# Kernel optimization log

Measured on AMD Instinct MI355X. Metric: run time of the kernel, lower is better.

## Reference

```python
import jax, jax.numpy as jnp
import numpy as np

N_NODES = 40000
N_EDGES = 640000
H = 128
N_REL2 = 474  # 2 * n_rel
BN_EPS = 1e-5


def setup_inputs() -> dict:
    key = jax.random.key(0)
    k1, k2, k3, k4, k5 = jax.random.split(key, 5)
    ent_emb = jax.random.normal(k1, (N_NODES, H), dtype=jnp.float32)
    rel_emb = jax.random.normal(k2, (N_REL2, H), dtype=jnp.float32)
    neigh_w = jax.random.normal(k3, (H, H), dtype=jnp.float32) * (1.0 / np.sqrt(H))
    bn_gamma = jnp.ones((H,), dtype=jnp.float32)
    bn_beta = jnp.zeros((H,), dtype=jnp.float32)
    rel_id = jax.random.randint(k4, (N_EDGES,), 0, N_REL2, dtype=jnp.int64)
    dst = jax.random.randint(k5, (N_EDGES,), 0, N_NODES, dtype=jnp.int64)
    return {"ent_emb": ent_emb, "rel_emb": rel_emb, "neigh_w": neigh_w,
            "bn_gamma": bn_gamma, "bn_beta": bn_beta, "rel_id": rel_id, "dst": dst}


def reference(ent_emb, rel_emb, neigh_w, bn_gamma, bn_beta, rel_id, dst):
    # per-edge relation embedding (gather)            [E, H]
    e = rel_emb[rel_id]
    # e_dot_v: edge emb dot destination node emb      [E]
    s = jnp.einsum('eh,eh->e', e, ent_emb[dst])
    # edge_softmax: softmax of s over edges grouped by destination node
    smax = jax.ops.segment_max(s, dst, num_segments=N_NODES)  # [N]
    ex = jnp.exp(s - smax[dst])
    denom = jax.ops.segment_sum(ex, dst, num_segments=N_NODES)  # [N]
    norm = ex / denom[dst]                                       # [E]
    # copy_e + sum: weighted scatter-sum of edge embeddings to dst nodes
    neigh = jax.ops.segment_sum(e * norm[:, None], dst, num_segments=N_NODES)  # [N, H]
    # dense update: mm + BatchNorm1d (training-mode batch stats) + tanh
    h = neigh @ neigh_w
    mean = jnp.mean(h, axis=0)
    var = jnp.var(h, axis=0)
    h = (h - mean) * jax.lax.rsqrt(var + BN_EPS) * bn_gamma + bn_beta
    return jnp.tanh(h)
```

## Files before the change

kernel.cpp:

```cpp
#include <hip/hip_runtime.h>

#define N_NODES 40000
#define N_EDGES 640000
#define HD 128
#define N_REL2 474
#define BN_EPS 1e-5f
#define NB_SCAN ((N_NODES + 255) / 256)

__global__ __launch_bounds__(256) void k_hist(
        const int* __restrict__ dst, int* __restrict__ counts) {
    int e = blockIdx.x * 256 + threadIdx.x;
    if (e < N_EDGES) atomicAdd(counts + dst[e], 1);
}

__global__ __launch_bounds__(256) void k_scan_part(
        const int* __restrict__ counts, int* __restrict__ bsum) {
    __shared__ int ls[256];
    int t = threadIdx.x;
    int idx = blockIdx.x * 256 + t;
    ls[t] = (idx < N_NODES) ? counts[idx] : 0;
    __syncthreads();
    #pragma unroll
    for (int off = 128; off > 0; off >>= 1) {
        if (t < off) ls[t] += ls[t + off];
        __syncthreads();
    }
    if (t == 0) bsum[blockIdx.x] = ls[0];
}

__global__ __launch_bounds__(256) void k_scan_down(
        const int* __restrict__ counts, const int* __restrict__ bsum,
        int* __restrict__ row_off, int* __restrict__ cursor) {
    __shared__ int btop[256];
    __shared__ int ls[256];
    int t = threadIdx.x;
    btop[t] = (t < NB_SCAN) ? bsum[t] : 0;
    __syncthreads();
    #pragma unroll
    for (int off = 1; off < 256; off <<= 1) {
        int tmp = (t >= off) ? btop[t - off] : 0;
        __syncthreads();
        btop[t] += tmp;
        __syncthreads();
    }
    int blockoff = (blockIdx.x == 0) ? 0 : btop[blockIdx.x - 1];
    int idx = blockIdx.x * 256 + t;
    int v = (idx < N_NODES) ? counts[idx] : 0;
    ls[t] = v;
    __syncthreads();
    #pragma unroll
    for (int off = 1; off < 256; off <<= 1) {
        int tmp = (t >= off) ? ls[t - off] : 0;
        __syncthreads();
        ls[t] += tmp;
        __syncthreads();
    }
    int excl = ls[t] - v + blockoff;
    if (idx < N_NODES) {
        row_off[idx] = excl;
        cursor[idx] = excl;
    }
    if (idx == N_NODES) row_off[N_NODES] = N_EDGES;
}

__global__ __launch_bounds__(256) void k_edge_sort(
        const float* __restrict__ ent_emb, const float* __restrict__ R,
        const int* __restrict__ rel_id, const int* __restrict__ dst,
        int* __restrict__ cursor, float2* __restrict__ sorted_pr) {
    int t = threadIdx.x;
    int e = blockIdx.x * 16 + (t >> 4);
    if (e >= N_EDGES) return;
    int lam = t & 15;
    int r = rel_id[e], d = dst[e];
    const float4* rr = (const float4*)(R + (size_t)r * HD);
    const float4* ee = (const float4*)(ent_emb + (size_t)d * HD);
    float4 a0 = rr[lam * 2], a1 = rr[lam * 2 + 1];
    float4 b0 = ee[lam * 2], b1 = ee[lam * 2 + 1];
    float s = a0.x * b0.x + a0.y * b0.y + a0.z * b0.z + a0.w * b0.w
            + a1.x * b1.x + a1.y * b1.y + a1.z * b1.z + a1.w * b1.w;
    #pragma unroll
    for (int m = 8; m >= 1; m >>= 1) s += __shfl_xor(s, m, 64);
    if (lam == 0) {
        float p = __expf(s);
        int pos = atomicAdd(cursor + d, 1);
        sorted_pr[pos] = make_float2(p, __int_as_float(r));
    }
}

__global__ __launch_bounds__(128) void k_rw(
        const float* __restrict__ R, const float* __restrict__ W,
        float* __restrict__ RW) {
    __shared__ float row[HD];
    int r = blockIdx.x, c = threadIdx.x;
    row[c] = R[(size_t)r * HD + c];
    __syncthreads();
    float acc = 0.f;
    #pragma unroll 8
    for (int k = 0; k < HD; ++k) acc += row[k] * W[(size_t)k * HD + c];
    RW[(size_t)r * HD + c] = acc;
}

__global__ __launch_bounds__(256) void k_node_acc(
        const float* __restrict__ RW, const int* __restrict__ row_off,
        const float2* __restrict__ sorted_pr, float* __restrict__ h) {
    __shared__ __align__(8) float2 pr_s[4][64];
    int wave = threadIdx.x >> 6, lane = threadIdx.x & 63;
    int n = blockIdx.x * 4 + wave;
    if (n >= N_NODES) return;
    int beg = row_off[n], end = row_off[n + 1];
    int c4 = lane & 15, g = lane >> 4;
    float acc[8] = {};
    float lp = 0.f;
    const float4* RW4 = (const float4*)RW;
    for (int base = beg; base < end; base += 64) {
        int cnt = min(64, end - base);
        if (lane < cnt) pr_s[wave][lane] = sorted_pr[base + lane];
        for (int j0 = 0; j0 < cnt; j0 += 4) {
            int eidx = j0 + g;
            if (eidx < cnt) {
                float2 v = pr_s[wave][eidx];
                float p = v.x;
                int r = __float_as_int(v.y);
                const float4* rowp = RW4 + (size_t)r * 32 + c4 * 2;
                float4 w0 = rowp[0], w1 = rowp[1];
                lp += p;
                acc[0] += p * w0.x; acc[1] += p * w0.y;
                acc[2] += p * w0.z; acc[3] += p * w0.w;
                acc[4] += p * w1.x; acc[5] += p * w1.y;
                acc[6] += p * w1.z; acc[7] += p * w1.w;
            }
        }
    }
    #pragma unroll
    for (int m = 16; m <= 32; m <<= 1) {
        lp += __shfl_xor(lp, m, 64);
        #pragma unroll
        for (int k = 0; k < 8; ++k) acc[k] += __shfl_xor(acc[k], m, 64);
    }
    float invl = (lp > 0.f) ? 1.f / lp : 0.f;
    if (g == 0) {
        float4* op = (float4*)(h + (size_t)n * HD + c4 * 8);
        op[0] = make_float4(acc[0] * invl, acc[1] * invl, acc[2] * invl, acc[3] * invl);
        op[1] = make_float4(acc[4] * invl, acc[5] * invl, acc[6] * invl, acc[7] * invl);
    }
}

__global__ __launch_bounds__(256) void k_stats(
        const float* __restrict__ Hout, float* __restrict__ colsum,
        float* __restrict__ colsumsq) {
    __shared__ float ls[256], lq[256];
    int t = threadIdx.x;
    int c = t & 127, half = t >> 7;
    int rbase = blockIdx.x * 64;
    float sum = 0.f, sq = 0.f;
    #pragma unroll 4
    for (int i = 0; i < 32; ++i) {
        int r = rbase + half + i * 2;
        float v = Hout[(size_t)r * HD + c];
        sum += v;
        sq += v * v;
    }
    ls[t] = sum;
    lq[t] = sq;
    __syncthreads();
    if (t < 128) {
        sum = ls[t] + ls[t + 128];
        sq = lq[t] + lq[t + 128];
        atomicAdd(colsum + c, sum);
        atomicAdd(colsumsq + c, sq);
    }
}

__global__ __launch_bounds__(256) void k_apply(
        float* __restrict__ Hout, const float* __restrict__ colsum,
        const float* __restrict__ colsumsq, const float* __restrict__ gamma,
        const float* __restrict__ beta) {
    int idx = blockIdx.x * 256 + threadIdx.x;
    if (idx >= N_NODES * HD / 4) return;
    int c0 = (idx * 4) & 127;
    float4 hv4 = ((const float4*)Hout)[idx];
    const float inv = 1.f / (float)N_NODES;
    float hv[4] = {hv4.x, hv4.y, hv4.z, hv4.w};
    float o[4];
    #pragma unroll
    for (int j = 0; j < 4; ++j) {
        int c = c0 + j;
        float mean = colsum[c] * inv;
        float var = colsumsq[c] * inv - mean * mean;
        float rstd = rsqrtf(var + BN_EPS);
        float x = (hv[j] - mean) * rstd * gamma[c] + beta[c];
        o[j] = 1.f - 2.f / (__expf(2.f * x) + 1.f);
    }
    ((float4*)Hout)[idx] = make_float4(o[0], o[1], o[2], o[3]);
}

extern "C" void kernel_launch(void* const* d_in, const int* in_sizes, int n_in,
                              void* d_out, int out_size, void* d_ws, size_t ws_size,
                              hipStream_t stream) {
    const float* ent_emb  = (const float*)d_in[0];
    const float* rel_emb  = (const float*)d_in[1];
    const float* neigh_w  = (const float*)d_in[2];
    const float* bn_gamma = (const float*)d_in[3];
    const float* bn_beta  = (const float*)d_in[4];
    const int*   rel_id   = (const int*)d_in[5];
    const int*   dst      = (const int*)d_in[6];
    float* out = (float*)d_out;

    int*      counts     = (int*)d_ws;
    float*    colsum     = (float*)d_ws + 40000;
    float*    colsumsq   = (float*)d_ws + 40128;
    int*      row_off    = (int*)d_ws + 40256;
    int*      cursor     = (int*)d_ws + 80257;
    float2*   sorted_pr  = (float2*)((float*)d_ws + 120258);
    float*    RW         = (float*)d_ws + 120258 + 2 * N_EDGES;
    int*      bsum       = (int*)d_ws + 120258 + 2 * N_EDGES + N_REL2 * HD;

    hipMemsetAsync(d_ws, 0, (size_t)40256 * 4, stream);

    k_hist<<<(N_EDGES + 255) / 256, 256, 0, stream>>>(dst, counts);
    k_scan_part<<<NB_SCAN, 256, 0, stream>>>(counts, bsum);
    k_scan_down<<<NB_SCAN, 256, 0, stream>>>(counts, bsum, row_off, cursor);
    k_edge_sort<<<N_EDGES / 16, 256, 0, stream>>>(ent_emb, rel_emb, rel_id, dst, cursor, sorted_pr);
    k_rw<<<N_REL2, 128, 0, stream>>>(rel_emb, neigh_w, RW);
    k_node_acc<<<N_NODES / 4, 256, 0, stream>>>(RW, row_off, sorted_pr, out);
    k_stats<<<N_NODES / 64, 256, 0, stream>>>(out, colsum, colsumsq);
    k_apply<<<N_NODES * HD / 4 / 256, 256, 0, stream>>>(out, colsum, colsumsq, bn_gamma, bn_beta);
}
```

Measured before the change: 157.4 us.

## Split edge scoring into a CSR scatter pass and a dst-sorted dot-product pass

Per-edge scoring is split into two passes. The first pass only scatters (rel_id, dst) pairs into CSR order with atomics. A separate kernel then computes the dot products in sorted order, so consecutive edges share the same destination row of ent_emb, which should improve cache locality. It also uses 4 lanes per edge instead of 16. The cost is an extra kernel launch plus writing and reading an extra 640K-entry int2 buffer.

```diff
diff --git a/kernel.cpp b/kernel.cpp
--- a/kernel.cpp
+++ b/kernel.cpp
@@ -63,27 +63,14 @@
     if (idx == N_NODES) row_off[N_NODES] = N_EDGES;
 }
 
-__global__ __launch_bounds__(256) void k_edge_sort(
-        const float* __restrict__ ent_emb, const float* __restrict__ R,
-        const int* __restrict__ rel_id, const int* __restrict__ dst,
-        int* __restrict__ cursor, float2* __restrict__ sorted_pr) {
-    int t = threadIdx.x;
-    int e = blockIdx.x * 16 + (t >> 4);
-    if (e >= N_EDGES) return;
-    int lam = t & 15;
-    int r = rel_id[e], d = dst[e];
-    const float4* rr = (const float4*)(R + (size_t)r * HD);
-    const float4* ee = (const float4*)(ent_emb + (size_t)d * HD);
-    float4 a0 = rr[lam * 2], a1 = rr[lam * 2 + 1];
-    float4 b0 = ee[lam * 2], b1 = ee[lam * 2 + 1];
-    float s = a0.x * b0.x + a0.y * b0.y + a0.z * b0.z + a0.w * b0.w
-            + a1.x * b1.x + a1.y * b1.y + a1.z * b1.z + a1.w * b1.w;
-    #pragma unroll
-    for (int m = 8; m >= 1; m >>= 1) s += __shfl_xor(s, m, 64);
-    if (lam == 0) {
-        float p = __expf(s);
-        int pos = atomicAdd(cursor + d, 1);
-        sorted_pr[pos] = make_float2(p, __int_as_float(r));
+__global__ __launch_bounds__(256) void k_sortrel(
+        const int* __restrict__ dst, const int* __restrict__ rel_id,
+        int* __restrict__ cursor, int2* __restrict__ sorted_rn) {
+    int e = blockIdx.x * 256 + threadIdx.x;
+    if (e < N_EDGES) {
+        int d = dst[e];
+        int p = atomicAdd(cursor + d, 1);
+        sorted_rn[p] = make_int2(rel_id[e], d);
     }
 }
 
@@ -98,6 +85,28 @@
     #pragma unroll 8
     for (int k = 0; k < HD; ++k) acc += row[k] * W[(size_t)k * HD + c];
     RW[(size_t)r * HD + c] = acc;
+}
+
+__global__ __launch_bounds__(256) void k_edge_dot(
+        const float* __restrict__ ent_emb, const float* __restrict__ R,
+        const int2* __restrict__ sorted_rn, float2* __restrict__ sorted_pr) {
+    int t = threadIdx.x;
+    int e = blockIdx.x * 64 + (t >> 2);
+    if (e >= N_EDGES) return;
+    int sub = t & 3;
+    int2 rn = sorted_rn[e];
+    const float4* rr = (const float4*)(R + (size_t)rn.x * HD);
+    const float4* ee = (const float4*)(ent_emb + (size_t)rn.y * HD);
+    float d = 0.f;
+    #pragma unroll
+    for (int k = 0; k < 8; ++k) {
+        float4 a = rr[sub * 8 + k];
+        float4 b = ee[sub * 8 + k];
+        d += a.x * b.x + a.y * b.y + a.z * b.z + a.w * b.w;
+    }
+    d += __shfl_xor(d, 1, 64);
+    d += __shfl_xor(d, 2, 64);
+    if (sub == 0) sorted_pr[e] = make_float2(__expf(d), __int_as_float(rn.x));
 }
 
 __global__ __launch_bounds__(256) void k_node_acc(
@@ -211,17 +220,19 @@
     float*    colsumsq   = (float*)d_ws + 40128;
     int*      row_off    = (int*)d_ws + 40256;
     int*      cursor     = (int*)d_ws + 80257;
-    float2*   sorted_pr  = (float2*)((float*)d_ws + 120258);
-    float*    RW         = (float*)d_ws + 120258 + 2 * N_EDGES;
-    int*      bsum       = (int*)d_ws + 120258 + 2 * N_EDGES + N_REL2 * HD;
+    int2*     sorted_rn  = (int2*)((float*)d_ws + 120258);
+    float2*   sorted_pr  = (float2*)((float*)d_ws + 1400258);
+    float*    RW         = (float*)d_ws + 2680258;
+    int*      bsum       = (int*)d_ws + 2680258 + N_REL2 * HD;
 
     hipMemsetAsync(d_ws, 0, (size_t)40256 * 4, stream);
 
     k_hist<<<(N_EDGES + 255) / 256, 256, 0, stream>>>(dst, counts);
     k_scan_part<<<NB_SCAN, 256, 0, stream>>>(counts, bsum);
     k_scan_down<<<NB_SCAN, 256, 0, stream>>>(counts, bsum, row_off, cursor);
-    k_edge_sort<<<N_EDGES / 16, 256, 0, stream>>>(ent_emb, rel_emb, rel_id, dst, cursor, sorted_pr);
+    k_sortrel<<<(N_EDGES + 255) / 256, 256, 0, stream>>>(dst, rel_id, cursor, sorted_rn);
     k_rw<<<N_REL2, 128, 0, stream>>>(rel_emb, neigh_w, RW);
+    k_edge_dot<<<N_EDGES / 64, 256, 0, stream>>>(ent_emb, rel_emb, sorted_rn, sorted_pr);
     k_node_acc<<<N_NODES / 4, 256, 0, stream>>>(RW, row_off, sorted_pr, out);
     k_stats<<<N_NODES / 64, 256, 0, stream>>>(out, colsum, colsumsq);
     k_apply<<<N_NODES * HD / 4 / 256, 256, 0, stream>>>(out, colsum, colsumsq, bn_gamma, bn_beta);
```

New measurement: 217.2 us. 1.38x slower.

## Use split-fp16 dot products and pack edge score with relation id

Applied to the files above, without the earlier changes.

Converts entity and relation embeddings into hi/lo fp16 pairs and computes the edge scores with fdot2 (three products per pair) instead of fp32 FMAs. Each edge's score is clamped, quantized to fixed point and packed with the relation id into one 32-bit word; the exp is moved into the node accumulation kernel. The counts buffer is reused as the cursor. The intent is to halve the sorted edge payload and use packed math, but it adds a full conversion pass over ent_emb, and the score clamp and quantization may reduce accuracy.

```diff
diff --git a/kernel.cpp b/kernel.cpp
--- a/kernel.cpp
+++ b/kernel.cpp
@@ -7,6 +7,16 @@
 #define BN_EPS 1e-5f
 #define NB_SCAN ((N_NODES + 255) / 256)
 
+typedef _Float16 half2_t __attribute__((ext_vector_type(2)));
+
+static __device__ __forceinline__ float dot2acc(half2_t a, half2_t b, float c) {
+#if __has_builtin(__builtin_amdgcn_fdot2)
+    return __builtin_amdgcn_fdot2(a, b, c, false);
+#else
+    return c + (float)a[0] * (float)b[0] + (float)a[1] * (float)b[1];
+#endif
+}
+
 __global__ __launch_bounds__(256) void k_hist(
         const int* __restrict__ dst, int* __restrict__ counts) {
     int e = blockIdx.x * 256 + threadIdx.x;
@@ -29,8 +39,8 @@
 }
 
 __global__ __launch_bounds__(256) void k_scan_down(
-        const int* __restrict__ counts, const int* __restrict__ bsum,
-        int* __restrict__ row_off, int* __restrict__ cursor) {
+        int* __restrict__ counts, const int* __restrict__ bsum,
+        int* __restrict__ row_off) {
     __shared__ int btop[256];
     __shared__ int ls[256];
     int t = threadIdx.x;
@@ -58,41 +68,40 @@
     int excl = ls[t] - v + blockoff;
     if (idx < N_NODES) {
         row_off[idx] = excl;
-        cursor[idx] = excl;
+        counts[idx] = excl;
     }
     if (idx == N_NODES) row_off[N_NODES] = N_EDGES;
 }
 
-__global__ __launch_bounds__(256) void k_edge_sort(
-        const float* __restrict__ ent_emb, const float* __restrict__ R,
-        const int* __restrict__ rel_id, const int* __restrict__ dst,
-        int* __restrict__ cursor, float2* __restrict__ sorted_pr) {
-    int t = threadIdx.x;
-    int e = blockIdx.x * 16 + (t >> 4);
-    if (e >= N_EDGES) return;
-    int lam = t & 15;
-    int r = rel_id[e], d = dst[e];
-    const float4* rr = (const float4*)(R + (size_t)r * HD);
-    const float4* ee = (const float4*)(ent_emb + (size_t)d * HD);
-    float4 a0 = rr[lam * 2], a1 = rr[lam * 2 + 1];
-    float4 b0 = ee[lam * 2], b1 = ee[lam * 2 + 1];
-    float s = a0.x * b0.x + a0.y * b0.y + a0.z * b0.z + a0.w * b0.w
-            + a1.x * b1.x + a1.y * b1.y + a1.z * b1.z + a1.w * b1.w;
-    #pragma unroll
-    for (int m = 8; m >= 1; m >>= 1) s += __shfl_xor(s, m, 64);
-    if (lam == 0) {
-        float p = __expf(s);
-        int pos = atomicAdd(cursor + d, 1);
-        sorted_pr[pos] = make_float2(p, __int_as_float(r));
-    }
+__global__ __launch_bounds__(256) void k_cvt_ent(
+        const float* __restrict__ ent, _Float16* __restrict__ ent_hl) {
+    int i = blockIdx.x * 256 + threadIdx.x;
+    if (i >= N_NODES * HD / 8) return;
+    int n = i >> 4, c8 = i & 15;
+    float4 a = ((const float4*)ent)[i * 2];
+    float4 b = ((const float4*)ent)[i * 2 + 1];
+    float v[8] = {a.x, a.y, a.z, a.w, b.x, b.y, b.z, b.w};
+    union { _Float16 h[8]; float4 f4; } hi, lo;
+    #pragma unroll
+    for (int k = 0; k < 8; ++k) {
+        _Float16 hh = (_Float16)v[k];
+        hi.h[k] = hh;
+        lo.h[k] = (_Float16)(v[k] - (float)hh);
+    }
+    *(float4*)(ent_hl + (size_t)n * 256 + c8 * 8) = hi.f4;
+    *(float4*)(ent_hl + (size_t)n * 256 + 128 + c8 * 8) = lo.f4;
 }
 
 __global__ __launch_bounds__(128) void k_rw(
         const float* __restrict__ R, const float* __restrict__ W,
-        float* __restrict__ RW) {
+        float* __restrict__ RW, _Float16* __restrict__ R_hl) {
     __shared__ float row[HD];
     int r = blockIdx.x, c = threadIdx.x;
-    row[c] = R[(size_t)r * HD + c];
+    float rv = R[(size_t)r * HD + c];
+    row[c] = rv;
+    _Float16 hh = (_Float16)rv;
+    R_hl[(size_t)r * 256 + c] = hh;
+    R_hl[(size_t)r * 256 + 128 + c] = (_Float16)(rv - (float)hh);
     __syncthreads();
     float acc = 0.f;
     #pragma unroll 8
@@ -100,10 +109,44 @@
     RW[(size_t)r * HD + c] = acc;
 }
 
+__global__ __launch_bounds__(256) void k_edge_all(
+        const _Float16* __restrict__ ent_hl, const _Float16* __restrict__ R_hl,
+        const int* __restrict__ rel_id, const int* __restrict__ dst,
+        int* __restrict__ cursor, unsigned* __restrict__ packed) {
+    int t = threadIdx.x;
+    int e = blockIdx.x * 16 + (t >> 4);
+    int lam = t & 15;
+    int r = rel_id[e], d = dst[e];
+    const float4* ap = (const float4*)(R_hl + (size_t)r * 256);
+    const float4* bp = (const float4*)(ent_hl + (size_t)d * 256);
+    float4 ah4 = ap[lam], al4 = ap[lam + 16];
+    float4 bh4 = bp[lam], bl4 = bp[lam + 16];
+    const half2_t* ah = (const half2_t*)&ah4;
+    const half2_t* al = (const half2_t*)&al4;
+    const half2_t* bh = (const half2_t*)&bh4;
+    const half2_t* bl = (const half2_t*)&bl4;
+    float s = 0.f;
+    #pragma unroll
+    for (int k = 0; k < 4; ++k) {
+        s = dot2acc(ah[k], bh[k], s);
+        s = dot2acc(ah[k], bl[k], s);
+        s = dot2acc(al[k], bh[k], s);
+    }
+    #pragma unroll
+    for (int m = 8; m >= 1; m >>= 1) s += __shfl_xor(s, m, 64);
+    if (lam == 0) {
+        float sc = fminf(fmaxf(s, -63.9f), 63.9f);
+        int si = (int)rintf(sc * 65536.f);
+        unsigned pkt = ((unsigned)r << 23) | ((unsigned)si & 0x7FFFFFu);
+        int pos = atomicAdd(cursor + d, 1);
+        packed[pos] = pkt;
+    }
+}
+
 __global__ __launch_bounds__(256) void k_node_acc(
         const float* __restrict__ RW, const int* __restrict__ row_off,
-        const float2* __restrict__ sorted_pr, float* __restrict__ h) {
-    __shared__ __align__(8) float2 pr_s[4][64];
+        const unsigned* __restrict__ packed, float* __restrict__ h) {
+    __shared__ unsigned pk_s[4][64];
     int wave = threadIdx.x >> 6, lane = threadIdx.x & 63;
     int n = blockIdx.x * 4 + wave;
     if (n >= N_NODES) return;
@@ -114,13 +157,14 @@
     const float4* RW4 = (const float4*)RW;
     for (int base = beg; base < end; base += 64) {
         int cnt = min(64, end - base);
-        if (lane < cnt) pr_s[wave][lane] = sorted_pr[base + lane];
+        if (lane < cnt) pk_s[wave][lane] = packed[base + lane];
         for (int j0 = 0; j0 < cnt; j0 += 4) {
             int eidx = j0 + g;
             if (eidx < cnt) {
-                float2 v = pr_s[wave][eidx];
-                float p = v.x;
-                int r = __float_as_int(v.y);
+                unsigned pkt = pk_s[wave][eidx];
+                int r = pkt >> 23;
+                float sv = (float)(((int)(pkt << 9)) >> 9) * (1.f / 65536.f);
+                float p = __expf(sv);
                 const float4* rowp = RW4 + (size_t)r * 32 + c4 * 2;
                 float4 w0 = rowp[0], w1 = rowp[1];
                 lp += p;
@@ -206,23 +250,25 @@
     const int*   dst      = (const int*)d_in[6];
     float* out = (float*)d_out;
 
-    int*      counts     = (int*)d_ws;
-    float*    colsum     = (float*)d_ws + 40000;
-    float*    colsumsq   = (float*)d_ws + 40128;
-    int*      row_off    = (int*)d_ws + 40256;
-    int*      cursor     = (int*)d_ws + 80257;
-    float2*   sorted_pr  = (float2*)((float*)d_ws + 120258);
-    float*    RW         = (float*)d_ws + 120258 + 2 * N_EDGES;
-    int*      bsum       = (int*)d_ws + 120258 + 2 * N_EDGES + N_REL2 * HD;
+    int*      counts  = (int*)d_ws;
+    float*    colsum  = (float*)d_ws + 40000;
+    float*    colsumsq= (float*)d_ws + 40128;
+    int*      row_off = (int*)d_ws + 40256;
+    unsigned* packed  = (unsigned*)d_ws + 80257;
+    float*    RW      = (float*)d_ws + 720260;
+    _Float16* R_hl    = (_Float16*)((float*)d_ws + 780932);
+    _Float16* ent_hl  = (_Float16*)((float*)d_ws + 841604);
+    int*      bsum    = (int*)d_ws + 5961604;
 
     hipMemsetAsync(d_ws, 0, (size_t)40256 * 4, stream);
 
     k_hist<<<(N_EDGES + 255) / 256, 256, 0, stream>>>(dst, counts);
     k_scan_part<<<NB_SCAN, 256, 0, stream>>>(counts, bsum);
-    k_scan_down<<<NB_SCAN, 256, 0, stream>>>(counts, bsum, row_off, cursor);
-    k_edge_sort<<<N_EDGES / 16, 256, 0, stream>>>(ent_emb, rel_emb, rel_id, dst, cursor, sorted_pr);
-    k_rw<<<N_REL2, 128, 0, stream>>>(rel_emb, neigh_w, RW);
-    k_node_acc<<<N_NODES / 4, 256, 0, stream>>>(RW, row_off, sorted_pr, out);
+    k_scan_down<<<NB_SCAN, 256, 0, stream>>>(counts, bsum, row_off);
+    k_cvt_ent<<<(N_NODES * HD / 8 + 255) / 256, 256, 0, stream>>>(ent_emb, ent_hl);
+    k_rw<<<N_REL2, 128, 0, stream>>>(rel_emb, neigh_w, RW, R_hl);
+    k_edge_all<<<N_EDGES / 16, 256, 0, stream>>>(ent_hl, R_hl, rel_id, dst, counts, packed);
+    k_node_acc<<<N_NODES / 4, 256, 0, stream>>>(RW, row_off, packed, out);
     k_stats<<<N_NODES / 64, 256, 0, stream>>>(out, colsum, colsumsq);
     k_apply<<<N_NODES * HD / 4 / 256, 256, 0, stream>>>(out, colsum, colsumsq, bn_gamma, bn_beta);
 }
```

After: 171.2 us. +8.8%, slower.
